# Optimization experiments

Measured on AMD Instinct MI355X. Metric: run time of the kernel, lower is better.

Reference implementation:

```python
import jax, jax.numpy as jnp
import numpy as np

H = 8           # hidden_size
IN = 1          # input_size
OUT = 1         # output_size
T_IN = 512      # input_length
T_OUT = 128     # output_length
B = 65536       # batch


def _gru_cell(x, h, W_ih, W_hh, b_ih, b_hh):
    # torch.nn.GRUCell math. x: [B, D], h: [B, H]
    gi = x @ W_ih.T + b_ih          # [B, 3H]
    gh = h @ W_hh.T + b_hh          # [B, 3H]
    i_r, i_z, i_n = jnp.split(gi, 3, axis=-1)
    h_r, h_z, h_n = jnp.split(gh, 3, axis=-1)
    r = jax.nn.sigmoid(i_r + h_r)
    z = jax.nn.sigmoid(i_z + h_z)
    n = jnp.tanh(i_n + r * h_n)
    return (1.0 - z) * n + z * h


def setup_inputs() -> dict:
    key = jax.random.key(0)
    ks = jax.random.split(key, 12)
    s_in = 1.0 / np.sqrt(H)
    x = jax.random.normal(ks[0], (T_IN, B, IN), dtype=jnp.float32)
    u = lambda k, shp: jax.random.uniform(k, shp, dtype=jnp.float32, minval=-s_in, maxval=s_in)
    return {
        "x": x,
        "enc_W_ih": u(ks[1], (3 * H, IN)),
        "enc_W_hh": u(ks[2], (3 * H, H)),
        "enc_b_ih": u(ks[3], (3 * H,)),
        "enc_b_hh": u(ks[4], (3 * H,)),
        "dec_W_ih": u(ks[5], (3 * H, OUT)),
        "dec_W_hh": u(ks[6], (3 * H, H)),
        "dec_b_ih": u(ks[7], (3 * H,)),
        "dec_b_hh": u(ks[8], (3 * H,)),
        "fc_W": u(ks[9], (OUT, H)),
        "fc_b": u(ks[10], (OUT,)),
    }


def reference(x, enc_W_ih, enc_W_hh, enc_b_ih, enc_b_hh,
              dec_W_ih, dec_W_hh, dec_b_ih, dec_b_hh, fc_W, fc_b):
    batch = x.shape[1]
    h0 = jnp.zeros((batch, H), dtype=x.dtype)

    def enc_step(h, x_t):
        return _gru_cell(x_t, h, enc_W_ih, enc_W_hh, enc_b_ih, enc_b_hh), None

    enc_h, _ = jax.lax.scan(enc_step, h0, x)

    def dec_step(carry, _):
        h, inp = carry
        h = _gru_cell(inp, h, dec_W_ih, dec_W_hh, dec_b_ih, dec_b_hh)
        out_t = h @ fc_W.T + fc_b      # [B, OUT]
        return (h, out_t), out_t

    # decoder_feat is None, teacher_forcing False: feed back own prediction
    _, outs = jax.lax.scan(dec_step, (enc_h, x[-1]), None, length=T_OUT)
    return outs  # [T_OUT, B, OUT]
```

## Files before the change

### kernel.cpp

```cpp
#include <hip/hip_runtime.h>

#define T_IN   512
#define T_OUT  128
#define BATCH  65536

typedef float v2f __attribute__((ext_vector_type(2)));

__device__ __forceinline__ float rcp_fast(float v) { return __builtin_amdgcn_rcpf(v); }
__device__ __forceinline__ float exp2_fast(float v) { return __builtin_amdgcn_exp2f(v); }

__device__ __forceinline__ v2f pk_fma(v2f a, v2f b, v2f c) {
    v2f d;
    asm("v_pk_fma_f32 %0, %1, %2, %3" : "=v"(d) : "v"(a), "v"(b), "v"(c));
    return d;
}
__device__ __forceinline__ void pk_fma_ip(v2f& acc, v2f a, v2f b) {
    asm("v_pk_fma_f32 %0, %1, %2, %0" : "+v"(acc) : "v"(a), "v"(b));
}
__device__ __forceinline__ v2f pk_mul(v2f a, v2f b) {
    v2f d;
    asm("v_pk_mul_f32 %0, %1, %2" : "=v"(d) : "v"(a), "v"(b));
    return d;
}
__device__ __forceinline__ v2f pk_add(v2f a, v2f b) {
    v2f d;
    asm("v_pk_add_f32 %0, %1, %2" : "=v"(d) : "v"(a), "v"(b));
    return d;
}
__device__ __forceinline__ void pk_fma_L(v2f& acc, v2f w, v2f h) {
    asm("v_pk_fma_f32 %0, %1, %2, %0 op_sel:[0,0,0] op_sel_hi:[1,0,1]"
        : "+v"(acc) : "v"(w), "v"(h));
}
__device__ __forceinline__ void pk_fma_H(v2f& acc, v2f w, v2f h) {
    asm("v_pk_fma_f32 %0, %1, %2, %0 op_sel:[0,1,0] op_sel_hi:[1,1,1]"
        : "+v"(acc) : "v"(w), "v"(h));
}
__device__ __forceinline__ v2f pk_fma_L0(v2f w, v2f h, v2f c) {
    v2f d;
    asm("v_pk_fma_f32 %0, %1, %2, %3 op_sel:[0,0,0] op_sel_hi:[1,0,1]"
        : "=v"(d) : "v"(w), "v"(h), "v"(c));
    return d;
}

template<int CTRL>
__device__ __forceinline__ float dppf(float v) {
    return __int_as_float(__builtin_amdgcn_mov_dpp(__float_as_int(v), CTRL, 0xF, 0xF, false));
}
#define QP_XOR1 0xB1
#define QP_XOR2 0x4E
#define QP_XOR3 0x1B

__global__ __launch_bounds__(256, 4) void gru_seq2seq(
    const float* __restrict__ x,
    const float* __restrict__ eWih, const float* __restrict__ eWhh,
    const float* __restrict__ eBih, const float* __restrict__ eBhh,
    const float* __restrict__ dWih, const float* __restrict__ dWhh,
    const float* __restrict__ dBih, const float* __restrict__ dBhh,
    const float* __restrict__ fcW,  const float* __restrict__ fcB,
    float* __restrict__ out)
{
    const int tid = threadIdx.x;
    const int u   = tid & 3;
    const int e0  = (int)blockIdx.x * 64 + (tid >> 2);

    const float CR = -1.44269504088896340736f;
    const float CN =  2.88539008177792681472f;

    const int r0 = 2*u, r1 = 2*u + 1;

    v2f wr[8], wz[8], wn[8];
    v2f wirp, wizp, winp;
    v2f brp, bzp, bnp, binp;

    auto load_w = [&](const float* Wih, const float* Whh,
                      const float* Bih, const float* Bhh) {
        #pragma unroll
        for (int m = 0; m < 4; ++m) {
            #pragma unroll
            for (int lh = 0; lh < 2; ++lh) {
                const int j = 2*(u^m) + lh;
                wr[2*m+lh] = v2f{ Whh[r0*8      + j] * CR, Whh[r1*8      + j] * CR };
                wz[2*m+lh] = v2f{ Whh[(r0+8)*8  + j] * CR, Whh[(r1+8)*8  + j] * CR };
                wn[2*m+lh] = v2f{ Whh[(r0+16)*8 + j] * CN, Whh[(r1+16)*8 + j] * CN };
            }
        }
        wirp = v2f{ Wih[r0]    * CR, Wih[r1]    * CR };
        wizp = v2f{ Wih[r0+8]  * CR, Wih[r1+8]  * CR };
        winp = v2f{ Wih[r0+16] * CN, Wih[r1+16] * CN };
        brp  = v2f{ (Bih[r0]   + Bhh[r0])   * CR, (Bih[r1]   + Bhh[r1])   * CR };
        bzp  = v2f{ (Bih[r0+8] + Bhh[r0+8]) * CR, (Bih[r1+8] + Bhh[r1+8]) * CR };
        bnp  = v2f{ Bhh[r0+16] * CN,              Bhh[r1+16] * CN };
        binp = v2f{ Bih[r0+16] * CN,              Bih[r1+16] * CN };
    };

    load_w(eWih, eWhh, eBih, eBhh);

    const v2f C_NEG2 = {-2.f, -2.f};
    const v2f C_ONE  = { 1.f,  1.f};
    const v2f C_HALF = { 0.5f, 0.5f};

    v2f hp[4];
    #pragma unroll
    for (int m = 0; m < 4; ++m) hp[m] = v2f{0.f, 0.f};

    auto cell = [&](v2f xv) {
        v2f ar = pk_fma_L0(wr[0], hp[0], brp);
        v2f az = pk_fma_L0(wz[0], hp[0], bzp);
        v2f an = pk_fma_L0(wn[0], hp[0], bnp);
        pk_fma_H(ar, wr[1], hp[0]);
        pk_fma_H(az, wz[1], hp[0]);
        pk_fma_H(an, wn[1], hp[0]);
        #pragma unroll
        for (int m = 1; m < 4; ++m) {
            pk_fma_L(ar, wr[2*m],   hp[m]);
            pk_fma_L(az, wz[2*m],   hp[m]);
            pk_fma_L(an, wn[2*m],   hp[m]);
            pk_fma_H(ar, wr[2*m+1], hp[m]);
            pk_fma_H(az, wz[2*m+1], hp[m]);
            pk_fma_H(an, wn[2*m+1], hp[m]);
        }
        const v2f sr = pk_fma(xv, wirp, ar);
        const v2f sz = pk_fma(xv, wizp, az);

        const float er0 = exp2_fast(sr.x), er1 = exp2_fast(sr.y);
        const float ez0 = exp2_fast(sz.x), ez1 = exp2_fast(sz.y);
        const float dr0 = 1.0f + er0, dr1 = 1.0f + er1;
        const float dz0 = 1.0f + ez0, dz1 = 1.0f + ez1;
        const float P0  = dr0 * dz0,  P1  = dr1 * dz1;
        const float rp  = rcp_fast(P0 * P1);
        const float rpA = rp * P1,    rpB = rp * P0;
        const v2f r01 = { dz0 * rpA, dz1 * rpB };
        const v2f z01 = { dr0 * rpA, dr1 * rpB };

        v2f pre = pk_fma(xv, winp, binp);
        pre = pk_fma(r01, an, pre);
        const float en0 = exp2_fast(pre.x), en1 = exp2_fast(pre.y);
        const float Dn0 = 1.0f + en0, Dn1 = 1.0f + en1;
        const float rpn = rcp_fast(Dn0 * Dn1);
        const v2f rn  = { rpn * Dn1, rpn * Dn0 };
        const v2f n01 = pk_fma(C_NEG2, rn, C_ONE);

        const v2f hm = pk_fma(n01, C_NEG2 * C_HALF , hp[0]);
        hp[0] = pk_fma(z01, hm, n01);

        const float g0 = hp[0].x, g1 = hp[0].y;
        hp[1] = v2f{ dppf<QP_XOR1>(g0), dppf<QP_XOR1>(g1) };
        hp[2] = v2f{ dppf<QP_XOR2>(g0), dppf<QP_XOR2>(g1) };
        hp[3] = v2f{ dppf<QP_XOR3>(g0), dppf<QP_XOR3>(g1) };
    };

    const float* xp = x + e0;
    float x0 = xp[0];
    float x1 = xp[BATCH];
    xp += 2 * (size_t)BATCH;
    #pragma unroll 2
    for (int t = 0; t < T_IN - 2; ++t) {
        const float x2 = *xp; xp += BATCH;
        cell(v2f{x0, x0});
        x0 = x1; x1 = x2;
    }
    cell(v2f{x0, x0});
    cell(v2f{x1, x1});

    load_w(dWih, dWhh, dBih, dBhh);
    const v2f fwp = v2f{ fcW[r0], fcW[r1] };
    const float fb = fcB[0];

    float inp = x1;
    float* outp = out + e0;
    #pragma unroll 1
    for (int t = 0; t < T_OUT; ++t) {
        cell(v2f{inp, inp});
        const v2f ay = pk_mul(fwp, hp[0]);
        float s = ay.x + ay.y;
        s += dppf<QP_XOR1>(s);
        s += dppf<QP_XOR2>(s);
        const float y = s + fb;
        if (u == 0) outp[t * BATCH] = y;
        inp = y;
    }
}

extern "C" void kernel_launch(void* const* d_in, const int* in_sizes, int n_in,
                              void* d_out, int out_size, void* d_ws, size_t ws_size,
                              hipStream_t stream) {
    const float* x    = (const float*)d_in[0];
    const float* eWih = (const float*)d_in[1];
    const float* eWhh = (const float*)d_in[2];
    const float* eBih = (const float*)d_in[3];
    const float* eBhh = (const float*)d_in[4];
    const float* dWih = (const float*)d_in[5];
    const float* dWhh = (const float*)d_in[6];
    const float* dBih = (const float*)d_in[7];
    const float* dBhh = (const float*)d_in[8];
    const float* fcW  = (const float*)d_in[9];
    const float* fcB  = (const float*)d_in[10];
    float* out = (float*)d_out;

    dim3 grid(BATCH / 64);
    dim3 block(256);
    gru_seq2seq<<<grid, block, 0, stream>>>(x, eWih, eWhh, eBih, eBhh,
                                            dWih, dWhh, dBih, dBhh,
                                            fcW, fcB, out);
}
```

Baseline: 345.2 us.

## Interleave two independent GRU batch elements per thread to hide latency

Each thread now advances two independent recurrent chains (elements e0 and e0+64) in lockstep, which halves the grid and lowers the launch-bounds occupancy hint to 2. The goal is instruction-level parallelism: the dependent FMA, exp and rcp chains of one chain can overlap with those of the other. The cost is higher register pressure and fewer waves for the hardware to switch between. Unused helpers were also removed, along with a constant-folding tweak.

```diff
diff --git a/kernel.cpp b/kernel.cpp
--- a/kernel.cpp
+++ b/kernel.cpp
@@ -14,17 +14,9 @@
     asm("v_pk_fma_f32 %0, %1, %2, %3" : "=v"(d) : "v"(a), "v"(b), "v"(c));
     return d;
 }
-__device__ __forceinline__ void pk_fma_ip(v2f& acc, v2f a, v2f b) {
-    asm("v_pk_fma_f32 %0, %1, %2, %0" : "+v"(acc) : "v"(a), "v"(b));
-}
 __device__ __forceinline__ v2f pk_mul(v2f a, v2f b) {
     v2f d;
     asm("v_pk_mul_f32 %0, %1, %2" : "=v"(d) : "v"(a), "v"(b));
-    return d;
-}
-__device__ __forceinline__ v2f pk_add(v2f a, v2f b) {
-    v2f d;
-    asm("v_pk_add_f32 %0, %1, %2" : "=v"(d) : "v"(a), "v"(b));
     return d;
 }
 __device__ __forceinline__ void pk_fma_L(v2f& acc, v2f w, v2f h) {
@@ -50,7 +42,7 @@
 #define QP_XOR2 0x4E
 #define QP_XOR3 0x1B
 
-__global__ __launch_bounds__(256, 4) void gru_seq2seq(
+__global__ __launch_bounds__(256, 2) void gru_seq2seq(
     const float* __restrict__ x,
     const float* __restrict__ eWih, const float* __restrict__ eWhh,
     const float* __restrict__ eBih, const float* __restrict__ eBhh,
@@ -61,7 +53,7 @@
 {
     const int tid = threadIdx.x;
     const int u   = tid & 3;
-    const int e0  = (int)blockIdx.x * 64 + (tid >> 2);
+    const int e0  = (int)blockIdx.x * 128 + (tid >> 2);
 
     const float CR = -1.44269504088896340736f;
     const float CN =  2.88539008177792681472f;
@@ -97,13 +89,14 @@
 
     const v2f C_NEG2 = {-2.f, -2.f};
     const v2f C_ONE  = { 1.f,  1.f};
-    const v2f C_HALF = { 0.5f, 0.5f};
-
-    v2f hp[4];
+    const v2f C_M1   = {-1.f, -1.f};
+
+    v2f hpA[4], hpB[4];
     #pragma unroll
-    for (int m = 0; m < 4; ++m) hp[m] = v2f{0.f, 0.f};
-
-    auto cell = [&](v2f xv) {
+    for (int m = 0; m < 4; ++m) { hpA[m] = v2f{0.f, 0.f}; hpB[m] = v2f{0.f, 0.f}; }
+
+    auto cell = [&](v2f (&hp)[4], float xs) {
+        const v2f xv = { xs, xs };
         v2f ar = pk_fma_L0(wr[0], hp[0], brp);
         v2f az = pk_fma_L0(wz[0], hp[0], bzp);
         v2f an = pk_fma_L0(wn[0], hp[0], bnp);
@@ -140,7 +133,7 @@
         const v2f rn  = { rpn * Dn1, rpn * Dn0 };
         const v2f n01 = pk_fma(C_NEG2, rn, C_ONE);
 
-        const v2f hm = pk_fma(n01, C_NEG2 * C_HALF , hp[0]);
+        const v2f hm = pk_fma(n01, C_M1, hp[0]);
         hp[0] = pk_fma(z01, hm, n01);
 
         const float g0 = hp[0].x, g1 = hp[0].y;
@@ -150,34 +143,48 @@
     };
 
     const float* xp = x + e0;
-    float x0 = xp[0];
-    float x1 = xp[BATCH];
+    float xa0 = xp[0],     xb0 = xp[64];
+    float xa1 = xp[BATCH], xb1 = xp[BATCH + 64];
     xp += 2 * (size_t)BATCH;
     #pragma unroll 2
     for (int t = 0; t < T_IN - 2; ++t) {
-        const float x2 = *xp; xp += BATCH;
-        cell(v2f{x0, x0});
-        x0 = x1; x1 = x2;
+        const float xa2 = xp[0];
+        const float xb2 = xp[64];
+        xp += BATCH;
+        cell(hpA, xa0);
+        cell(hpB, xb0);
+        xa0 = xa1; xa1 = xa2;
+        xb0 = xb1; xb1 = xb2;
     }
-    cell(v2f{x0, x0});
-    cell(v2f{x1, x1});
+    cell(hpA, xa0); cell(hpB, xb0);
+    cell(hpA, xa1); cell(hpB, xb1);
 
     load_w(dWih, dWhh, dBih, dBhh);
     const v2f fwp = v2f{ fcW[r0], fcW[r1] };
     const float fb = fcB[0];
 
-    float inp = x1;
+    float inpA = xa1, inpB = xb1;
     float* outp = out + e0;
     #pragma unroll 1
     for (int t = 0; t < T_OUT; ++t) {
-        cell(v2f{inp, inp});
-        const v2f ay = pk_mul(fwp, hp[0]);
-        float s = ay.x + ay.y;
-        s += dppf<QP_XOR1>(s);
-        s += dppf<QP_XOR2>(s);
-        const float y = s + fb;
-        if (u == 0) outp[t * BATCH] = y;
-        inp = y;
+        cell(hpA, inpA);
+        cell(hpB, inpB);
+        const v2f ayA = pk_mul(fwp, hpA[0]);
+        const v2f ayB = pk_mul(fwp, hpB[0]);
+        float sA = ayA.x + ayA.y;
+        float sB = ayB.x + ayB.y;
+        sA += dppf<QP_XOR1>(sA);
+        sB += dppf<QP_XOR1>(sB);
+        sA += dppf<QP_XOR2>(sA);
+        sB += dppf<QP_XOR2>(sB);
+        const float yA = sA + fb;
+        const float yB = sB + fb;
+        if (u == 0) {
+            outp[t * BATCH]      = yA;
+            outp[t * BATCH + 64] = yB;
+        }
+        inpA = yA;
+        inpB = yB;
     }
 }
 
@@ -197,7 +204,7 @@
     const float* fcB  = (const float*)d_in[10];
     float* out = (float*)d_out;
 
-    dim3 grid(BATCH / 64);
+    dim3 grid(BATCH / 128);
     dim3 block(256);
     gru_seq2seq<<<grid, block, 0, stream>>>(x, eWih, eWhh, eBih, eBhh,
                                             dWih, dWhh, dBih, dBhh,
```

New measurement: 376.2 us. 9.0% more time.
